# Kernel optimization log

Hardware: AMD Instinct MI355X
Metric: run time of the kernel (lower is better)

Reference implementation:

```python
import jax, jax.numpy as jnp
import numpy as np

N = 100000
E = 2000000
LN_EPS = 1e-5


def _ln(x, g, b):
    m = jnp.mean(x, axis=-1, keepdims=True)
    v = jnp.mean((x - m) ** 2, axis=-1, keepdims=True)
    return (x - m) * jax.lax.rsqrt(v + LN_EPS) * g + b


def _gcn_conv(x, W, b, row, col, n_nodes):
    xw = x @ W  # [N, out_dim]
    deg = jax.ops.segment_sum(jnp.ones((row.shape[0],), xw.dtype), row, num_segments=n_nodes) + 1.0
    dinv = jax.lax.rsqrt(deg)
    norm = dinv[row] * dinv[col]  # [E]
    msg = xw[col] * norm[:, None]  # gather + scale, [E, out_dim]
    agg = jax.ops.segment_sum(msg, row, num_segments=n_nodes)
    self_loop = xw * (dinv * dinv)[:, None]
    return agg + self_loop + b


def setup_inputs() -> dict:
    key = jax.random.key(0)
    ks = jax.random.split(key, 32)
    s = 0.05
    d = dict(
        coords=jax.random.normal(ks[0], (N, 2), jnp.float32),
        features=jax.random.normal(ks[1], (N, 3), jnp.float32),
        edge_index=jax.random.randint(ks[2], (2, E), 0, N, jnp.int32),
        # spatial encoder FFN: 2->128, two hidden 128->128 (relu+LN), last 128->128 (relu)
        fw0=jax.random.normal(ks[3], (2, 128), jnp.float32) * s,
        fb0=jnp.zeros((128,), jnp.float32),
        fg0=jnp.ones((128,), jnp.float32),
        fe0=jnp.zeros((128,), jnp.float32),
        fw1=jax.random.normal(ks[4], (128, 128), jnp.float32) * s,
        fb1=jnp.zeros((128,), jnp.float32),
        fg1=jnp.ones((128,), jnp.float32),
        fe1=jnp.zeros((128,), jnp.float32),
        fw2=jax.random.normal(ks[5], (128, 128), jnp.float32) * s,
        fb2=jnp.zeros((128,), jnp.float32),
        fg2=jnp.ones((128,), jnp.float32),
        fe2=jnp.zeros((128,), jnp.float32),
        fw3=jax.random.normal(ks[6], (128, 128), jnp.float32) * s,
        fb3=jnp.zeros((128,), jnp.float32),
        # dec: 128->64->32->16 with tanh between
        dw0=jax.random.normal(ks[7], (128, 64), jnp.float32) * s,
        db0=jnp.zeros((64,), jnp.float32),
        dw1=jax.random.normal(ks[8], (64, 32), jnp.float32) * s,
        db1=jnp.zeros((32,), jnp.float32),
        dw2=jax.random.normal(ks[9], (32, 16), jnp.float32) * s,
        db2=jnp.zeros((16,), jnp.float32),
        # GCN convs: (3+16)->64, 64->64; fc 64->1
        cw1=jax.random.normal(ks[10], (19, 64), jnp.float32) * s,
        cb1=jnp.zeros((64,), jnp.float32),
        cw2=jax.random.normal(ks[11], (64, 64), jnp.float32) * s,
        cb2=jnp.zeros((64,), jnp.float32),
        ow=jax.random.normal(ks[12], (64, 1), jnp.float32) * s,
        ob=jnp.zeros((1,), jnp.float32),
    )
    return d


def reference(coords, features, edge_index,
              fw0, fb0, fg0, fe0, fw1, fb1, fg1, fe1, fw2, fb2, fg2, fe2, fw3, fb3,
              dw0, db0, dw1, db1, dw2, db2,
              cw1, cb1, cw2, cb2, ow, ob):
    # positional encoder FFN (dropout disabled / eval mode)
    h = _ln(jax.nn.relu(coords @ fw0 + fb0), fg0, fe0)
    h = _ln(jax.nn.relu(h @ fw1 + fb1), fg1, fe1)
    h = _ln(jax.nn.relu(h @ fw2 + fb2), fg2, fe2)
    h = jax.nn.relu(h @ fw3 + fb3)
    # decoder to emb_dim
    emb = jnp.tanh(h @ dw0 + db0)
    emb = jnp.tanh(emb @ dw1 + db1)
    emb = emb @ dw2 + db2  # [N, 16]
    x = jnp.concatenate([features, emb], axis=-1)  # [N, 19]
    row, col = edge_index[0], edge_index[1]
    h1 = jax.nn.relu(_gcn_conv(x, cw1, cb1, row, col, x.shape[0]))
    h2 = _gcn_conv(h1, cw2, cb2, row, col, x.shape[0])
    out = h2 @ ow + ob  # [N, 1]
    return out
```

## Files before the change

### kernel.cpp

```cpp
#include <hip/hip_runtime.h>
#include <hip/hip_bf16.h>
#include <math.h>

#define TM 64
#define XROW 64

typedef float v2f __attribute__((ext_vector_type(2)));
typedef float f32x4 __attribute__((ext_vector_type(4)));
typedef __bf16 bf16x8 __attribute__((ext_vector_type(8)));
typedef unsigned short u16x8 __attribute__((ext_vector_type(8)));
typedef unsigned int uint_t;
typedef unsigned short ushort_t;

__device__ __forceinline__ v2f fma2(v2f a, v2f b, v2f c) {
    return __builtin_elementwise_fma(a, b, c);
}
__device__ __forceinline__ v2f splat2(float s) { return (v2f){s, s}; }
__device__ __forceinline__ v2f max02(v2f a) {
    return (v2f){fmaxf(a.x, 0.0f), fmaxf(a.y, 0.0f)};
}
__device__ __forceinline__ uint_t pack_bf16(float lo, float hi) {
    uint_t r;
    asm volatile("v_cvt_pk_bf16_f32 %0, %1, %2" : "=v"(r) : "v"(lo), "v"(hi));
    return r;
}
__device__ __forceinline__ float bf16_f(ushort_t u) {
    union { uint_t i; float f; } c; c.i = ((uint_t)u) << 16; return c.f;
}
__device__ __forceinline__ float blo(uint_t u) {
    union { uint_t i; float f; } c; c.i = u << 16; return c.f;
}
__device__ __forceinline__ float bhi(uint_t u) {
    union { uint_t i; float f; } c; c.i = u & 0xffff0000u; return c.f;
}

__device__ __forceinline__ int aaddr(int node, int feat) {
    return (node * 256 + feat * 2) ^ ((node & 15) << 4);
}

__global__ void prepw_kernel(const float* __restrict__ W, ushort_t* __restrict__ out,
                             int K, int N) {
    int idx = blockIdx.x * 256 + threadIdx.x;
    int total = 2 * K * N;
    if (idx >= total) return;
    int j    = idx & 7;
    int lane = (idx >> 3) & 63;
    int rest = idx >> 9;
    int ncb  = N >> 4;
    int cb   = rest % ncb;
    int r2   = rest / ncb;
    int nkk  = K >> 5;
    int kk   = r2 % nkk;
    int h    = r2 / nkk;
    int k = kk * 32 + (lane >> 4) * 8 + j;
    int n = cb * 16 + (lane & 15);
    float wv = W[k * N + n];
    ushort_t hi = (ushort_t)pack_bf16(wv, wv);
    if (h == 0) {
        out[idx] = hi;
    } else {
        float res = wv - bf16_f(hi);
        out[idx] = (ushort_t)pack_bf16(res, res);
    }
}

__global__ __launch_bounds__(256, 4) void ffn_kernel(
    const float* __restrict__ coords, const float* __restrict__ features,
    const float* __restrict__ dinv,
    const float* __restrict__ fw0, const float* __restrict__ fb0,
    const float* __restrict__ fg0, const float* __restrict__ fe0,
    const ushort_t* __restrict__ wswz,
    const float* __restrict__ fb1, const float* __restrict__ fg1, const float* __restrict__ fe1,
    const float* __restrict__ fb2, const float* __restrict__ fg2, const float* __restrict__ fe2,
    const float* __restrict__ fb3,
    const float* __restrict__ dw0, const float* __restrict__ db0,
    const float* __restrict__ dw1, const float* __restrict__ db1,
    const float* __restrict__ dw2, const float* __restrict__ db2,
    char* __restrict__ xsb, int n_nodes)
{
    __shared__ __align__(16) char abuf[16384];
    __shared__ ushort_t tbuf[128][64];
    __shared__ float ps1[4][64];
    __shared__ float ps2[4][64];

    const int t    = threadIdx.x;
    const int lane = t & 63;
    const int w    = __builtin_amdgcn_readfirstlane(t >> 6);
    const int jw   = w * 32;
    const int n0   = blockIdx.x * TM;

    int g = n0 + lane;
    if (g >= n_nodes) g = n_nodes - 1;

    {
        v2f acc[16];
        float2 c = *(const float2*)&coords[(size_t)g * 2];
        v2f cx = splat2(c.x), cy = splat2(c.y);
        #pragma unroll
        for (int q = 0; q < 16; q++) {
            int j = jw + 2 * q;
            v2f w0 = *(const v2f*)&fw0[j];
            v2f w1 = *(const v2f*)&fw0[128 + j];
            v2f bb = *(const v2f*)&fb0[j];
            acc[q] = max02(fma2(cx, w0, fma2(cy, w1, bb)));
        }
        float s1 = 0.f, s2 = 0.f;
        #pragma unroll
        for (int q = 0; q < 16; q++) {
            s1 += acc[q].x + acc[q].y;
            s2 += acc[q].x * acc[q].x + acc[q].y * acc[q].y;
        }
        ps1[w][lane] = s1; ps2[w][lane] = s2;
        __syncthreads();
        float t1 = ps1[0][lane] + ps1[1][lane] + ps1[2][lane] + ps1[3][lane];
        float t2 = ps2[0][lane] + ps2[1][lane] + ps2[2][lane] + ps2[3][lane];
        float mean = t1 * (1.0f / 128.0f);
        float var  = t2 * (1.0f / 128.0f) - mean * mean;
        float inv  = rsqrtf(var + 1e-5f);
        v2f mean2 = splat2(mean), inv2 = splat2(inv);
        #pragma unroll
        for (int q = 0; q < 16; q++) {
            int j = jw + 2 * q;
            v2f gm = *(const v2f*)&fg0[j];
            v2f bt = *(const v2f*)&fe0[j];
            v2f o = fma2((acc[q] - mean2) * inv2, gm, bt);
            *(uint_t*)(abuf + aaddr(lane, j)) = pack_bf16(o.x, o.y);
        }
        __syncthreads();
    }

    auto mfma_layer = [&](const ushort_t* Wb, const float* __restrict__ bias) {
        f32x4 acc[2][4] = {};
        #pragma unroll
        for (int kk = 0; kk < 4; kk++) {
            bf16x8 B[2][2];
            #pragma unroll
            for (int cb2 = 0; cb2 < 2; cb2++) {
                int cb = 2 * w + cb2;
                #pragma unroll
                for (int h = 0; h < 2; h++) {
                    const ushort_t* p = Wb + (size_t)(((h * 4 + kk) * 8 + cb) * 64 + lane) * 8;
                    B[cb2][h] = *(const bf16x8*)p;
                }
            }
            #pragma unroll
            for (int rb = 0; rb < 4; rb++) {
                int node = rb * 16 + (lane & 15);
                bf16x8 A = *(const bf16x8*)(abuf + aaddr(node, kk * 32 + (lane >> 4) * 8));
                #pragma unroll
                for (int cb2 = 0; cb2 < 2; cb2++) {
                    acc[cb2][rb] = __builtin_amdgcn_mfma_f32_16x16x32_bf16(A, B[cb2][0], acc[cb2][rb], 0, 0, 0);
                    acc[cb2][rb] = __builtin_amdgcn_mfma_f32_16x16x32_bf16(A, B[cb2][1], acc[cb2][rb], 0, 0, 0);
                }
            }
        }
        __syncthreads();
        float bv0 = bias[jw + (lane & 15)];
        float bv1 = bias[jw + 16 + (lane & 15)];
        #pragma unroll
        for (int cb2 = 0; cb2 < 2; cb2++) {
            int col = jw + cb2 * 16 + (lane & 15);
            float bv = cb2 ? bv1 : bv0;
            #pragma unroll
            for (int rb = 0; rb < 4; rb++) {
                #pragma unroll
                for (int r = 0; r < 4; r++) {
                    float v = fmaxf(acc[cb2][rb][r] + bv, 0.0f);
                    int node = rb * 16 + (lane >> 4) * 4 + r;
                    *(ushort_t*)(abuf + aaddr(node, col)) = (ushort_t)pack_bf16(v, v);
                }
            }
        }
        __syncthreads();
    };

    auto ln_pass = [&](const float* __restrict__ gam, const float* __restrict__ bet) {
        int node = t >> 2;
        int part = t & 3;
        float vals[32];
        float s1 = 0.f, s2 = 0.f;
        #pragma unroll
        for (int q = 0; q < 4; q++) {
            int f0 = part * 32 + q * 8;
            u16x8 u = *(const u16x8*)(abuf + aaddr(node, f0));
            #pragma unroll
            for (int i = 0; i < 8; i++) {
                float v = bf16_f(u[i]);
                vals[q * 8 + i] = v;
                s1 += v; s2 += v * v;
            }
        }
        s1 += __shfl_xor(s1, 1); s1 += __shfl_xor(s1, 2);
        s2 += __shfl_xor(s2, 1); s2 += __shfl_xor(s2, 2);
        float mean = s1 * (1.0f / 128.0f);
        float var  = s2 * (1.0f / 128.0f) - mean * mean;
        float inv  = rsqrtf(var + 1e-5f);
        #pragma unroll
        for (int q = 0; q < 4; q++) {
            int f0 = part * 32 + q * 8;
            uint_t ov[4];
            #pragma unroll
            for (int p = 0; p < 4; p++) {
                v2f gm = *(const v2f*)&gam[f0 + 2 * p];
                v2f bt = *(const v2f*)&bet[f0 + 2 * p];
                float a = (vals[q * 8 + 2 * p]     - mean) * inv * gm.x + bt.x;
                float b = (vals[q * 8 + 2 * p + 1] - mean) * inv * gm.y + bt.y;
                ov[p] = pack_bf16(a, b);
            }
            uint4 uv = make_uint4(ov[0], ov[1], ov[2], ov[3]);
            *(uint4*)(abuf + aaddr(node, f0)) = uv;
        }
        __syncthreads();
    };

    mfma_layer(wswz,             fb1); ln_pass(fg1, fe1);
    mfma_layer(wswz + 32768,     fb2); ln_pass(fg2, fe2);
    mfma_layer(wswz + 65536,     fb3);

    {
        #pragma unroll
        for (int q = 0; q < 4; q++) {
            int f0 = jw + q * 8;
            u16x8 u = *(const u16x8*)(abuf + aaddr(lane, f0));
            #pragma unroll
            for (int i = 0; i < 8; i++) tbuf[f0 + i][lane] = u[i];
        }
        __syncthreads();
    }

    {
        const int j16 = w * 16;
        v2f d0[8];
        #pragma unroll
        for (int q = 0; q < 8; q++) d0[q] = *(const v2f*)&db0[j16 + 2 * q];
        #pragma unroll 4
        for (int k = 0; k < 128; k++) {
            v2f av = splat2(bf16_f(tbuf[k][lane]));
            const v2f* W2 = (const v2f*)(dw0 + k * 64 + j16);
            #pragma unroll
            for (int q = 0; q < 8; q++) d0[q] = fma2(av, W2[q], d0[q]);
        }
        #pragma unroll
        for (int q = 0; q < 8; q++) d0[q] = (v2f){tanhf(d0[q].x), tanhf(d0[q].y)};
        __syncthreads();
        #pragma unroll
        for (int q = 0; q < 8; q++) {
            uint_t r = pack_bf16(d0[q].x, d0[q].y);
            tbuf[j16 + 2 * q][lane]     = (ushort_t)r;
            tbuf[j16 + 2 * q + 1][lane] = (ushort_t)(r >> 16);
        }
        __syncthreads();
    }

    {
        const int j8 = w * 8;
        v2f d1[4];
        #pragma unroll
        for (int q = 0; q < 4; q++) d1[q] = *(const v2f*)&db1[j8 + 2 * q];
        #pragma unroll 4
        for (int k = 0; k < 64; k++) {
            v2f av = splat2(bf16_f(tbuf[k][lane]));
            const v2f* W2 = (const v2f*)(dw1 + k * 32 + j8);
            #pragma unroll
            for (int q = 0; q < 4; q++) d1[q] = fma2(av, W2[q], d1[q]);
        }
        #pragma unroll
        for (int q = 0; q < 4; q++) d1[q] = (v2f){tanhf(d1[q].x), tanhf(d1[q].y)};
        __syncthreads();
        #pragma unroll
        for (int q = 0; q < 4; q++) {
            uint_t r = pack_bf16(d1[q].x, d1[q].y);
            tbuf[j8 + 2 * q][lane]     = (ushort_t)r;
            tbuf[j8 + 2 * q + 1][lane] = (ushort_t)(r >> 16);
        }
        __syncthreads();
    }

    {
        const int j4 = w * 4;
        v2f d2[2];
        #pragma unroll
        for (int q = 0; q < 2; q++) d2[q] = *(const v2f*)&db2[j4 + 2 * q];
        #pragma unroll 4
        for (int k = 0; k < 32; k++) {
            v2f av = splat2(bf16_f(tbuf[k][lane]));
            const v2f* W2 = (const v2f*)(dw2 + k * 16 + j4);
            d2[0] = fma2(av, W2[0], d2[0]);
            d2[1] = fma2(av, W2[1], d2[1]);
        }
        __syncthreads();
        #pragma unroll
        for (int q = 0; q < 2; q++) {
            uint_t r = pack_bf16(d2[q].x, d2[q].y);
            tbuf[j4 + 2 * q][lane]     = (ushort_t)r;
            tbuf[j4 + 2 * q + 1][lane] = (ushort_t)(r >> 16);
        }
        __syncthreads();
    }

    {
        const int nn = t & 63;
        const int jg = t >> 6;
        int gg = n0 + nn;
        if (gg < n_nodes && jg < 3) {
            float dgg = dinv[gg];
            char* rp = xsb + (size_t)gg * XROW;
            if (jg == 0) {
                float4 f;
                f.x = features[(size_t)gg * 3 + 0] * dgg;
                f.y = features[(size_t)gg * 3 + 1] * dgg;
                f.z = features[(size_t)gg * 3 + 2] * dgg;
                f.w = 0.0f;
                *(float4*)rp = f;
            } else {
                int e0 = (jg - 1) * 8;
                uint_t u[4];
                #pragma unroll
                for (int p = 0; p < 4; p++) {
                    float lo = bf16_f(tbuf[e0 + 2 * p][nn]) * dgg;
                    float hi = bf16_f(tbuf[e0 + 2 * p + 1][nn]) * dgg;
                    u[p] = pack_bf16(lo, hi);
                }
                uint4 uv = make_uint4(u[0], u[1], u[2], u[3]);
                *(uint4*)(rp + 16 + (jg - 1) * 16) = uv;
            }
        }
    }
}

__global__ void deg_kernel(const int* __restrict__ row, int* __restrict__ cnt, int E_) {
    int e4 = (blockIdx.x * blockDim.x + threadIdx.x) * 4;
    if (e4 + 3 < E_) {
        int4 r = *(const int4*)&row[e4];
        atomicAdd(&cnt[r.x], 1); atomicAdd(&cnt[r.y], 1);
        atomicAdd(&cnt[r.z], 1); atomicAdd(&cnt[r.w], 1);
    } else {
        for (int e = e4; e < E_; e++) atomicAdd(&cnt[row[e]], 1);
    }
}

__global__ void scan1_kernel(const int* __restrict__ cnt, int* __restrict__ offs,
                             int* __restrict__ bsum, int n) {
    __shared__ int tmp[256];
    int t = threadIdx.x, b = blockIdx.x, i = b * 256 + t;
    int v = (i < n) ? cnt[i] : 0;
    tmp[t] = v; __syncthreads();
    #pragma unroll
    for (int d = 1; d < 256; d <<= 1) {
        int add = (t >= d) ? tmp[t - d] : 0;
        __syncthreads();
        tmp[t] += add;
        __syncthreads();
    }
    if (i < n) offs[i] = tmp[t] - v;
    if (t == 255) bsum[b] = tmp[t];
}

__global__ void scan2_kernel(int* __restrict__ bsum, int B) {
    __shared__ int tmp[512];
    int t = threadIdx.x;
    tmp[t] = (t < B) ? bsum[t] : 0; __syncthreads();
    #pragma unroll
    for (int d = 1; d < 512; d <<= 1) {
        int add = (t >= d) ? tmp[t - d] : 0;
        __syncthreads();
        tmp[t] += add;
        __syncthreads();
    }
    if (t < B) bsum[t] = tmp[t];
}

__global__ void scan3_kernel(int* __restrict__ offs, const int* __restrict__ bsum,
                             const int* __restrict__ cnt, int* __restrict__ fill,
                             float* __restrict__ dinv, int n) {
    int i = blockIdx.x * blockDim.x + threadIdx.x;
    if (i >= n) return;
    int b = i >> 8;
    int base = (b > 0) ? bsum[b - 1] : 0;
    int o = offs[i] + base;
    offs[i] = o;
    fill[i] = o;
    dinv[i] = rsqrtf((float)cnt[i] + 1.0f);
}

__global__ void scatter_kernel(const int* __restrict__ row, const int* __restrict__ col,
                               int* __restrict__ fill, int* __restrict__ es, int E_) {
    int e4 = (blockIdx.x * blockDim.x + threadIdx.x) * 4;
    if (e4 + 3 < E_) {
        int4 r = *(const int4*)&row[e4];
        int4 c = *(const int4*)&col[e4];
        es[atomicAdd(&fill[r.x], 1)] = c.x;
        es[atomicAdd(&fill[r.y], 1)] = c.y;
        es[atomicAdd(&fill[r.z], 1)] = c.z;
        es[atomicAdd(&fill[r.w], 1)] = c.w;
    } else {
        for (int e = e4; e < E_; e++) {
            int p = atomicAdd(&fill[row[e]], 1);
            es[p] = col[e];
        }
    }
}

__global__ void prep_kernel(const float* __restrict__ cw2, const float* __restrict__ cb2,
                            const float* __restrict__ ow, const float* __restrict__ ob,
                            float* __restrict__ wb) {
    int i = threadIdx.x;
    if (i < 64) {
        float a = 0.f;
        for (int j = 0; j < 64; j++) a += cw2[i * 64 + j] * ow[j];
        wb[i] = a;
    }
    if (i == 0) {
        float bb = 0.f;
        for (int j = 0; j < 64; j++) bb += cb2[j] * ow[j];
        wb[64] = bb + ob[0];
    }
}

__global__ __launch_bounds__(256) void node1g_kernel(
    const int* __restrict__ offs, const int* __restrict__ cnt, const int* __restrict__ es,
    const float* __restrict__ dinv, const char* __restrict__ xsb,
    const float* __restrict__ cw1, const float* __restrict__ cb1,
    const float* __restrict__ wb, float* __restrict__ ss, int n)
{
    __shared__ float w[19 * 64];
    __shared__ float bbs[64];
    __shared__ float wes[64];
    for (int i = threadIdx.x; i < 19 * 64; i += 256) w[i] = cw1[i];
    for (int i = threadIdx.x; i < 64; i += 256) { bbs[i] = cb1[i]; wes[i] = wb[i]; }
    __syncthreads();
    const int t  = threadIdx.x;
    const int oc = t & 7;
    const int i  = blockIdx.x * 32 + (t >> 3);
    if (i >= n) return;
    const float di = dinv[i];

    float af[19];
    #pragma unroll
    for (int q = 0; q < 19; q++) af[q] = 0.f;

    auto addrow = [&](const char* rp) {
        float4 F = *(const float4*)rp;
        uint4 U0 = *(const uint4*)(rp + 16);
        uint4 U1 = *(const uint4*)(rp + 32);
        af[0] += F.x; af[1] += F.y; af[2] += F.z;
        af[3]  += blo(U0.x); af[4]  += bhi(U0.x);
        af[5]  += blo(U0.y); af[6]  += bhi(U0.y);
        af[7]  += blo(U0.z); af[8]  += bhi(U0.z);
        af[9]  += blo(U0.w); af[10] += bhi(U0.w);
        af[11] += blo(U1.x); af[12] += bhi(U1.x);
        af[13] += blo(U1.y); af[14] += bhi(U1.y);
        af[15] += blo(U1.z); af[16] += bhi(U1.z);
        af[17] += blo(U1.w); af[18] += bhi(U1.w);
    };

    if (oc == 0) addrow(xsb + (size_t)i * XROW);
    const int st = offs[i], dg = cnt[i];
    for (int e = oc; e < dg; e += 8) {
        int c = es[st + e];
        addrow(xsb + (size_t)c * XROW);
    }

    float a19[19];
    #pragma unroll
    for (int q = 0; q < 19; q++) {
        float v = af[q];
        v += __shfl_xor(v, 1);
        v += __shfl_xor(v, 2);
        v += __shfl_xor(v, 4);
        a19[q] = v * di;
    }

    const int j0 = oc * 8;
    v2f am[4];
    const v2f* w2  = (const v2f*)w;
    const v2f* bb2 = (const v2f*)bbs;
    #pragma unroll
    for (int q = 0; q < 4; q++) am[q] = bb2[j0 / 2 + q];
    #pragma unroll
    for (int k = 0; k < 19; k++) {
        v2f v = splat2(a19[k]);
        #pragma unroll
        for (int q = 0; q < 4; q++) am[q] = fma2(v, w2[k * 32 + j0 / 2 + q], am[q]);
    }
    const v2f* we2 = (const v2f*)wes;
    v2f sv2 = {0.f, 0.f};
    #pragma unroll
    for (int q = 0; q < 4; q++) sv2 = fma2(max02(am[q]), we2[j0 / 2 + q], sv2);
    float sv = sv2.x + sv2.y;
    sv += __shfl_xor(sv, 1);
    sv += __shfl_xor(sv, 2);
    sv += __shfl_xor(sv, 4);
    if (oc == 0) ss[i] = di * sv;
}

__global__ __launch_bounds__(256) void outg_kernel(
    const int* __restrict__ offs, const int* __restrict__ cnt, const int* __restrict__ es,
    const float* __restrict__ dinv, const float* __restrict__ ss,
    const float* __restrict__ wb, float* __restrict__ out, int n)
{
    const int t  = threadIdx.x;
    const int oc = t & 7;
    const int i  = blockIdx.x * 32 + (t >> 3);
    if (i >= n) return;
    const int st = offs[i], dg = cnt[i];
    float sum = (oc == 0) ? ss[i] : 0.f;
    for (int e = oc; e < dg; e += 8) {
        int c = es[st + e];
        sum += ss[c];
    }
    sum += __shfl_xor(sum, 1);
    sum += __shfl_xor(sum, 2);
    sum += __shfl_xor(sum, 4);
    if (oc == 0) out[i] = wb[64] + dinv[i] * sum;
}

extern "C" void kernel_launch(void* const* d_in, const int* in_sizes, int n_in,
                              void* d_out, int out_size, void* d_ws, size_t ws_size,
                              hipStream_t stream) {
    const float* coords   = (const float*)d_in[0];
    const float* features = (const float*)d_in[1];
    const int*   eidx     = (const int*)d_in[2];
    const float* fw0 = (const float*)d_in[3];
    const float* fb0 = (const float*)d_in[4];
    const float* fg0 = (const float*)d_in[5];
    const float* fe0 = (const float*)d_in[6];
    const float* fw1 = (const float*)d_in[7];
    const float* fb1 = (const float*)d_in[8];
    const float* fg1 = (const float*)d_in[9];
    const float* fe1 = (const float*)d_in[10];
    const float* fw2 = (const float*)d_in[11];
    const float* fb2 = (const float*)d_in[12];
    const float* fg2 = (const float*)d_in[13];
    const float* fe2 = (const float*)d_in[14];
    const float* fw3 = (const float*)d_in[15];
    const float* fb3 = (const float*)d_in[16];
    const float* dw0 = (const float*)d_in[17];
    const float* db0 = (const float*)d_in[18];
    const float* dw1 = (const float*)d_in[19];
    const float* db1 = (const float*)d_in[20];
    const float* dw2 = (const float*)d_in[21];
    const float* db2 = (const float*)d_in[22];
    const float* cw1 = (const float*)d_in[23];
    const float* cb1 = (const float*)d_in[24];
    const float* cw2 = (const float*)d_in[25];
    const float* cb2 = (const float*)d_in[26];
    const float* ow  = (const float*)d_in[27];
    const float* ob  = (const float*)d_in[28];
    float* out = (float*)d_out;

    const int Nn = in_sizes[0] / 2;
    const int E_ = in_sizes[2] / 2;
    const int NB = (Nn + 255) / 256;
    const int NO = (Nn * 8 + 255) / 256;
    const int NT = (Nn + TM - 1) / TM;

    char* ws = (char*)d_ws;
    size_t o = 0;
    char*  xsb  = (char*) (ws + o); o += (size_t)Nn * XROW;
    int*   cnt  = (int*)  (ws + o); o += (size_t)Nn * sizeof(int);
    int*   offs = (int*)  (ws + o); o += (size_t)Nn * sizeof(int);
    int*   fill = (int*)  (ws + o); o += (size_t)Nn * sizeof(int);
    int*   bsum = (int*)  (ws + o); o += 512 * sizeof(int);
    float* dinv = (float*)(ws + o); o += (size_t)Nn * sizeof(float);
    float* ssb  = (float*)(ws + o); o += (size_t)Nn * sizeof(float);
    int*   es   = (int*)  (ws + o); o += (size_t)E_ * sizeof(int);
    float* wb   = (float*)(ws + o); o += 80 * sizeof(float);
    o = (o + 15) & ~(size_t)15;
    ushort_t* wswz = (ushort_t*)(ws + o); o += 3 * 32768 * sizeof(ushort_t);

    hipMemsetAsync(cnt, 0, (size_t)Nn * sizeof(int), stream);

    prepw_kernel<<<(32768 + 255) / 256, 256, 0, stream>>>(fw1, wswz,         128, 128);
    prepw_kernel<<<(32768 + 255) / 256, 256, 0, stream>>>(fw2, wswz + 32768, 128, 128);
    prepw_kernel<<<(32768 + 255) / 256, 256, 0, stream>>>(fw3, wswz + 65536, 128, 128);

    deg_kernel<<<(E_ / 4 + 255) / 256, 256, 0, stream>>>(eidx, cnt, E_);
    scan1_kernel<<<NB, 256, 0, stream>>>(cnt, offs, bsum, Nn);
    scan2_kernel<<<1, 512, 0, stream>>>(bsum, NB);
    scan3_kernel<<<NB, 256, 0, stream>>>(offs, bsum, cnt, fill, dinv, Nn);
    scatter_kernel<<<(E_ / 4 + 255) / 256, 256, 0, stream>>>(eidx, eidx + E_, fill, es, E_);

    ffn_kernel<<<NT, 256, 0, stream>>>(
        coords, features, dinv,
        fw0, fb0, fg0, fe0,
        wswz,
        fb1, fg1, fe1, fb2, fg2, fe2, fb3,
        dw0, db0, dw1, db1, dw2, db2, xsb, Nn);

    prep_kernel<<<1, 64, 0, stream>>>(cw2, cb2, ow, ob, wb);
    node1g_kernel<<<NO, 256, 0, stream>>>(offs, cnt, es, dinv, xsb, cw1, cb1, wb, ssb, Nn);
    outg_kernel<<<NO, 256, 0, stream>>>(offs, cnt, es, dinv, ssb, wb, out, Nn);
}
```

Before: 430.1 us.

## Split degree counters into 8 segments to cut atomic contention in CSR build

```diff
diff --git a/kernel.cpp b/kernel.cpp
--- a/kernel.cpp
+++ b/kernel.cpp
@@ -4,6 +4,7 @@
 
 #define TM 64
 #define XROW 64
+#define NSEG 8
 
 typedef float v2f __attribute__((ext_vector_type(2)));
 typedef float f32x4 __attribute__((ext_vector_type(4)));
@@ -213,9 +214,9 @@
         __syncthreads();
     };
 
-    mfma_layer(wswz,             fb1); ln_pass(fg1, fe1);
-    mfma_layer(wswz + 32768,     fb2); ln_pass(fg2, fe2);
-    mfma_layer(wswz + 65536,     fb3);
+    mfma_layer(wswz,         fb1); ln_pass(fg1, fe1);
+    mfma_layer(wswz + 32768, fb2); ln_pass(fg2, fe2);
+    mfma_layer(wswz + 65536, fb3);
 
     {
         #pragma unroll
@@ -328,23 +329,33 @@
     }
 }
 
-__global__ void deg_kernel(const int* __restrict__ row, int* __restrict__ cnt, int E_) {
+__global__ void deg8_kernel(const int* __restrict__ row, int* __restrict__ cnt8,
+                            int E_, int Nn) {
+    int s = blockIdx.x & (NSEG - 1);
+    int* cs = cnt8 + (size_t)s * Nn;
     int e4 = (blockIdx.x * blockDim.x + threadIdx.x) * 4;
     if (e4 + 3 < E_) {
         int4 r = *(const int4*)&row[e4];
-        atomicAdd(&cnt[r.x], 1); atomicAdd(&cnt[r.y], 1);
-        atomicAdd(&cnt[r.z], 1); atomicAdd(&cnt[r.w], 1);
+        atomicAdd(&cs[r.x], 1); atomicAdd(&cs[r.y], 1);
+        atomicAdd(&cs[r.z], 1); atomicAdd(&cs[r.w], 1);
     } else {
-        for (int e = e4; e < E_; e++) atomicAdd(&cnt[row[e]], 1);
-    }
-}
-
-__global__ void scan1_kernel(const int* __restrict__ cnt, int* __restrict__ offs,
+        for (int e = e4; e < E_; e++) atomicAdd(&cs[row[e]], 1);
+    }
+}
+
+__global__ void scan1_kernel(const int* __restrict__ in, int* __restrict__ out,
                              int* __restrict__ bsum, int n) {
     __shared__ int tmp[256];
-    int t = threadIdx.x, b = blockIdx.x, i = b * 256 + t;
-    int v = (i < n) ? cnt[i] : 0;
-    tmp[t] = v; __syncthreads();
+    int t = threadIdx.x, b = blockIdx.x;
+    int base = b * 2048 + t * 8;
+    int v[8]; int s = 0;
+    #pragma unroll
+    for (int q = 0; q < 8; q++) {
+        int idx = base + q;
+        v[q] = (idx < n) ? in[idx] : 0;
+        s += v[q];
+    }
+    tmp[t] = s; __syncthreads();
     #pragma unroll
     for (int d = 1; d < 256; d <<= 1) {
         int add = (t >= d) ? tmp[t - d] : 0;
@@ -352,7 +363,13 @@
         tmp[t] += add;
         __syncthreads();
     }
-    if (i < n) offs[i] = tmp[t] - v;
+    int run = tmp[t] - s;
+    #pragma unroll
+    for (int q = 0; q < 8; q++) {
+        int idx = base + q;
+        if (idx < n) out[idx] = run;
+        run += v[q];
+    }
     if (t == 255) bsum[b] = tmp[t];
 }
 
@@ -370,32 +387,38 @@
     if (t < B) bsum[t] = tmp[t];
 }
 
-__global__ void scan3_kernel(int* __restrict__ offs, const int* __restrict__ bsum,
-                             const int* __restrict__ cnt, int* __restrict__ fill,
-                             float* __restrict__ dinv, int n) {
-    int i = blockIdx.x * blockDim.x + threadIdx.x;
+__global__ void scanfix_kernel(int* __restrict__ data, const int* __restrict__ bsum, int n) {
+    int i = blockIdx.x * 256 + threadIdx.x;
     if (i >= n) return;
-    int b = i >> 8;
-    int base = (b > 0) ? bsum[b - 1] : 0;
-    int o = offs[i] + base;
-    offs[i] = o;
-    fill[i] = o;
-    dinv[i] = rsqrtf((float)cnt[i] + 1.0f);
+    int b = i >> 11;
+    if (b > 0) data[i] += bsum[b - 1];
+}
+
+__global__ void dinv_kernel(const int* __restrict__ cnt8, float* __restrict__ dinv, int Nn) {
+    int i = blockIdx.x * 256 + threadIdx.x;
+    if (i >= Nn) return;
+    int s = 0;
+    #pragma unroll
+    for (int q = 0; q < NSEG; q++) s += cnt8[(size_t)q * Nn + i];
+    dinv[i] = rsqrtf((float)s + 1.0f);
 }
 
 __global__ void scatter_kernel(const int* __restrict__ row, const int* __restrict__ col,
-                               int* __restrict__ fill, int* __restrict__ es, int E_) {
+                               int* __restrict__ fill8, int* __restrict__ es,
+                               int E_, int Nn) {
+    int s = blockIdx.x & (NSEG - 1);
+    int* fs = fill8 + (size_t)s * Nn;
     int e4 = (blockIdx.x * blockDim.x + threadIdx.x) * 4;
     if (e4 + 3 < E_) {
         int4 r = *(const int4*)&row[e4];
         int4 c = *(const int4*)&col[e4];
-        es[atomicAdd(&fill[r.x], 1)] = c.x;
-        es[atomicAdd(&fill[r.y], 1)] = c.y;
-        es[atomicAdd(&fill[r.z], 1)] = c.z;
-        es[atomicAdd(&fill[r.w], 1)] = c.w;
+        es[atomicAdd(&fs[r.x], 1)] = c.x;
+        es[atomicAdd(&fs[r.y], 1)] = c.y;
+        es[atomicAdd(&fs[r.z], 1)] = c.z;
+        es[atomicAdd(&fs[r.w], 1)] = c.w;
     } else {
         for (int e = e4; e < E_; e++) {
-            int p = atomicAdd(&fill[row[e]], 1);
+            int p = atomicAdd(&fs[row[e]], 1);
             es[p] = col[e];
         }
     }
@@ -418,7 +441,7 @@
 }
 
 __global__ __launch_bounds__(256) void node1g_kernel(
-    const int* __restrict__ offs, const int* __restrict__ cnt, const int* __restrict__ es,
+    const int* __restrict__ fill8, const int* __restrict__ cnt8, const int* __restrict__ es,
     const float* __restrict__ dinv, const char* __restrict__ xsb,
     const float* __restrict__ cw1, const float* __restrict__ cb1,
     const float* __restrict__ wb, float* __restrict__ ss, int n)
@@ -455,9 +478,10 @@
     };
 
     if (oc == 0) addrow(xsb + (size_t)i * XROW);
-    const int st = offs[i], dg = cnt[i];
-    for (int e = oc; e < dg; e += 8) {
-        int c = es[st + e];
+    const int end = fill8[(size_t)oc * n + i];
+    const int dgs = cnt8[(size_t)oc * n + i];
+    for (int e = end - dgs; e < end; e++) {
+        int c = es[e];
         addrow(xsb + (size_t)c * XROW);
     }
 
@@ -495,7 +519,7 @@
 }
 
 __global__ __launch_bounds__(256) void outg_kernel(
-    const int* __restrict__ offs, const int* __restrict__ cnt, const int* __restrict__ es,
+    const int* __restrict__ fill8, const int* __restrict__ cnt8, const int* __restrict__ es,
     const float* __restrict__ dinv, const float* __restrict__ ss,
     const float* __restrict__ wb, float* __restrict__ out, int n)
 {
@@ -503,10 +527,11 @@
     const int oc = t & 7;
     const int i  = blockIdx.x * 32 + (t >> 3);
     if (i >= n) return;
-    const int st = offs[i], dg = cnt[i];
+    const int end = fill8[(size_t)oc * n + i];
+    const int dgs = cnt8[(size_t)oc * n + i];
     float sum = (oc == 0) ? ss[i] : 0.f;
-    for (int e = oc; e < dg; e += 8) {
-        int c = es[st + e];
+    for (int e = end - dgs; e < end; e++) {
+        int c = es[e];
         sum += ss[c];
     }
     sum += __shfl_xor(sum, 1);
@@ -551,35 +576,37 @@
 
     const int Nn = in_sizes[0] / 2;
     const int E_ = in_sizes[2] / 2;
-    const int NB = (Nn + 255) / 256;
+    const int n8 = NSEG * Nn;
+    const int NBS = (n8 + 2047) / 2048;
     const int NO = (Nn * 8 + 255) / 256;
     const int NT = (Nn + TM - 1) / TM;
+    const int NE = (E_ / 4 + 255) / 256;
 
     char* ws = (char*)d_ws;
     size_t o = 0;
-    char*  xsb  = (char*) (ws + o); o += (size_t)Nn * XROW;
-    int*   cnt  = (int*)  (ws + o); o += (size_t)Nn * sizeof(int);
-    int*   offs = (int*)  (ws + o); o += (size_t)Nn * sizeof(int);
-    int*   fill = (int*)  (ws + o); o += (size_t)Nn * sizeof(int);
-    int*   bsum = (int*)  (ws + o); o += 512 * sizeof(int);
-    float* dinv = (float*)(ws + o); o += (size_t)Nn * sizeof(float);
-    float* ssb  = (float*)(ws + o); o += (size_t)Nn * sizeof(float);
-    int*   es   = (int*)  (ws + o); o += (size_t)E_ * sizeof(int);
-    float* wb   = (float*)(ws + o); o += 80 * sizeof(float);
+    char*  xsb   = (char*) (ws + o); o += (size_t)Nn * XROW;
+    int*   cnt8  = (int*)  (ws + o); o += (size_t)n8 * sizeof(int);
+    int*   fill8 = (int*)  (ws + o); o += (size_t)n8 * sizeof(int);
+    int*   bsum  = (int*)  (ws + o); o += 512 * sizeof(int);
+    float* dinv  = (float*)(ws + o); o += (size_t)Nn * sizeof(float);
+    float* ssb   = (float*)(ws + o); o += (size_t)Nn * sizeof(float);
+    int*   es    = (int*)  (ws + o); o += (size_t)E_ * sizeof(int);
+    float* wb    = (float*)(ws + o); o += 80 * sizeof(float);
     o = (o + 15) & ~(size_t)15;
     ushort_t* wswz = (ushort_t*)(ws + o); o += 3 * 32768 * sizeof(ushort_t);
 
-    hipMemsetAsync(cnt, 0, (size_t)Nn * sizeof(int), stream);
+    hipMemsetAsync(cnt8, 0, (size_t)n8 * sizeof(int), stream);
 
     prepw_kernel<<<(32768 + 255) / 256, 256, 0, stream>>>(fw1, wswz,         128, 128);
     prepw_kernel<<<(32768 + 255) / 256, 256, 0, stream>>>(fw2, wswz + 32768, 128, 128);
     prepw_kernel<<<(32768 + 255) / 256, 256, 0, stream>>>(fw3, wswz + 65536, 128, 128);
 
-    deg_kernel<<<(E_ / 4 + 255) / 256, 256, 0, stream>>>(eidx, cnt, E_);
-    scan1_kernel<<<NB, 256, 0, stream>>>(cnt, offs, bsum, Nn);
-    scan2_kernel<<<1, 512, 0, stream>>>(bsum, NB);
-    scan3_kernel<<<NB, 256, 0, stream>>>(offs, bsum, cnt, fill, dinv, Nn);
-    scatter_kernel<<<(E_ / 4 + 255) / 256, 256, 0, stream>>>(eidx, eidx + E_, fill, es, E_);
+    deg8_kernel<<<NE, 256, 0, stream>>>(eidx, cnt8, E_, Nn);
+    scan1_kernel<<<NBS, 256, 0, stream>>>(cnt8, fill8, bsum, n8);
+    scan2_kernel<<<1, 512, 0, stream>>>(bsum, NBS);
+    scanfix_kernel<<<(n8 + 255) / 256, 256, 0, stream>>>(fill8, bsum, n8);
+    dinv_kernel<<<(Nn + 255) / 256, 256, 0, stream>>>(cnt8, dinv, Nn);
+    scatter_kernel<<<NE, 256, 0, stream>>>(eidx, eidx + E_, fill8, es, E_, Nn);
 
     ffn_kernel<<<NT, 256, 0, stream>>>(
         coords, features, dinv,
@@ -589,6 +616,6 @@
         dw0, db0, dw1, db1, dw2, db2, xsb, Nn);
 
     prep_kernel<<<1, 64, 0, stream>>>(cw2, cb2, ow, ob, wb);
-    node1g_kernel<<<NO, 256, 0, stream>>>(offs, cnt, es, dinv, xsb, cw1, cb1, wb, ssb, Nn);
-    outg_kernel<<<NO, 256, 0, stream>>>(offs, cnt, es, dinv, ssb, wb, out, Nn);
-}
+    node1g_kernel<<<NO, 256, 0, stream>>>(fill8, cnt8, es, dinv, xsb, cw1, cb1, wb, ssb, Nn);
+    outg_kernel<<<NO, 256, 0, stream>>>(fill8, cnt8, es, dinv, ssb, wb, out, Nn);
+}
```

Result: faster. 374.2 us (-13.0%).
